# Kernel optimization log

Measured on AMD Instinct MI355X. Metric: run time of the kernel, lower is better.

Reference implementation:

```python
import jax, jax.numpy as jnp
import numpy as np

N_NODES = 50000
N_EDGES = 600000
F_IN = 128
HID = 128
N_CLASSES = 10


def _gcn_graph(edge_index, n_nodes):
    # PyG GCNConv: add self-loops, deg computed on target (col) with weight 1,
    # norm_e = deg^-1/2[src] * deg^-1/2[dst]
    src = jnp.concatenate([edge_index[0], jnp.arange(n_nodes, dtype=edge_index.dtype)])
    dst = jnp.concatenate([edge_index[1], jnp.arange(n_nodes, dtype=edge_index.dtype)])
    deg = jax.ops.segment_sum(jnp.ones_like(dst, dtype=jnp.float32), dst, num_segments=n_nodes)
    dinv = jnp.where(deg > 0, jax.lax.rsqrt(deg), 0.0)
    norm = dinv[src] * dinv[dst]  # [E+N]
    return src, dst, norm


def _gcn_layer(x, W, b, src, dst, norm, n_nodes):
    h = x @ W                      # [N, out] linear first (bias applied post-agg)
    m = h[src] * norm[:, None]     # gather + scale, [E+N, out]
    out = jax.ops.segment_sum(m, dst, num_segments=n_nodes)  # scatter-add
    return out + b


def setup_inputs() -> dict:
    key = jax.random.key(0)
    ks = jax.random.split(key, 4)
    x = jax.random.normal(ks[0], (N_NODES, F_IN), dtype=jnp.float32)
    edge_index = jax.random.randint(ks[1], (2, N_EDGES), 0, N_NODES, dtype=jnp.int64)
    # Glorot-ish init scale for weights
    W_stack = jax.random.normal(ks[2], (8, HID, HID), dtype=jnp.float32) * (1.0 / np.sqrt(HID))
    b_stack = jnp.zeros((8, HID), dtype=jnp.float32)
    W_out = jax.random.normal(ks[3], (HID, N_CLASSES), dtype=jnp.float32) * (1.0 / np.sqrt(HID))
    b_out = jnp.zeros((N_CLASSES,), dtype=jnp.float32)
    return {"x": x, "edge_index": edge_index, "W_stack": W_stack, "b_stack": b_stack,
            "W_out": W_out, "b_out": b_out}


def reference(x, edge_index, W_stack, b_stack, W_out, b_out):
    n_nodes = x.shape[0]
    src, dst, norm = _gcn_graph(edge_index, n_nodes)
    h = x
    for i in range(8):  # conv1..conv8 with ELU
        h = jax.nn.elu(_gcn_layer(h, W_stack[i], b_stack[i], src, dst, norm, n_nodes))
    # conv9: no activation
    return _gcn_layer(h, W_out, b_out, src, dst, norm, n_nodes)
```

## Files before the change

kernel.cpp:

```cpp
#include <hip/hip_runtime.h>
#include <math.h>

#define NN 50000
#define NE 600000
#define HID 128
#define NCLS 10
#define T2S 16

typedef __bf16 bf16x8 __attribute__((ext_vector_type(8)));
typedef float f32x16 __attribute__((ext_vector_type(16)));

__device__ __forceinline__ void split3(float f, ushort& h, ushort& m, ushort& l) {
    unsigned uh = __float_as_uint(f) & 0xffff0000u;
    float fm = f - __uint_as_float(uh);
    unsigned um = __float_as_uint(fm) & 0xffff0000u;
    float fl = fm - __uint_as_float(um);
    h = (ushort)(uh >> 16);
    m = (ushort)(um >> 16);
    l = (ushort)(__float_as_uint(fl) >> 16);
}


__global__ __launch_bounds__(256) void k_count(const int* __restrict__ edge,
                                               int* __restrict__ counts) {
    int e = blockIdx.x * 256 + threadIdx.x;
    if (e < NE) atomicAdd(&counts[edge[NE + e]], 1);
}

__device__ __forceinline__ int wave_incl_scan(int x, int lane) {
#pragma unroll
    for (int off = 1; off < 64; off <<= 1) {
        int y = __shfl_up(x, off, 64);
        if (lane >= off) x += y;
    }
    return x;
}

__global__ __launch_bounds__(256) void k_scan1(const int* __restrict__ counts,
                                               int* __restrict__ rowptr,
                                               int* __restrict__ bsum,
                                               float* __restrict__ dinv) {
    __shared__ int ws[4];
    int tid = threadIdx.x;
    int i = blockIdx.x * 256 + tid;
    int lane = tid & 63, wv = tid >> 6;
    int v = (i < NN) ? counts[i] : 0;
    if (i < NN) dinv[i] = rsqrtf((float)(v + 1));
    int x = wave_incl_scan(v, lane);
    if (lane == 63) ws[wv] = x;
    __syncthreads();
    int off = 0;
    for (int j = 0; j < wv; ++j) off += ws[j];
    if (i < NN) rowptr[i] = off + x - v;
    if (tid == 255) bsum[blockIdx.x] = off + x;
}

__global__ __launch_bounds__(256) void k_scan2(int* __restrict__ bsum, int n) {
    __shared__ int ws[4];
    int tid = threadIdx.x;
    int lane = tid & 63, wv = tid >> 6;
    int v = (tid < n) ? bsum[tid] : 0;
    int x = wave_incl_scan(v, lane);
    if (lane == 63) ws[wv] = x;
    __syncthreads();
    int off = 0;
    for (int j = 0; j < wv; ++j) off += ws[j];
    __syncthreads();
    if (tid < n) bsum[tid] = off + x - v;
}

__global__ __launch_bounds__(256) void k_scan3(int* __restrict__ rowptr,
                                               const int* __restrict__ bsum) {
    int i = blockIdx.x * 256 + threadIdx.x;
    if (i < NN) rowptr[i] += bsum[blockIdx.x];
    if (i == 0) rowptr[NN] = NE;
}

__global__ __launch_bounds__(256) void k_fill(const int* __restrict__ edge,
                                              const int* __restrict__ rowptr,
                                              int* __restrict__ cursor,
                                              const float* __restrict__ dinv,
                                              int2* __restrict__ csr) {
    int e = blockIdx.x * 256 + threadIdx.x;
    if (e >= NE) return;
    int s = edge[e], d = edge[NE + e];
    int slot = atomicSub(&cursor[d], 1) - 1;
    csr[rowptr[d] + slot] = make_int2(s, __float_as_int(dinv[s] * dinv[d]));
}


__global__ __launch_bounds__(256) void k_split_w(const float* __restrict__ Wst,
                                                 ushort* __restrict__ Wt4) {
    int i = blockIdx.x * 256 + threadIdx.x;
    if (i >= 8 * HID * HID) return;
    int l = i >> 14;
    int k = (i >> 7) & 127;
    int n = i & 127;
    ushort h, m, lo;
    split3(Wst[i], h, m, lo);
    int ks = k >> 4, r = k & 15;
    size_t base = ((((size_t)l * 3) * 8 + ks) * 128 + n) * 16 + r;
    const size_t pstride = (size_t)8 * 128 * 16;
    Wt4[base] = h;
    Wt4[base + pstride] = m;
    Wt4[base + 2 * pstride] = lo;
}


__global__ __launch_bounds__(256) void k_mfma_gemm(const float* __restrict__ H,
                                                   const ushort* __restrict__ Wt,
                                                   float* __restrict__ T) {
    int tid = threadIdx.x;
    int lane = tid & 63, w = tid >> 6;
    int l31 = lane & 31, lh = lane >> 5;
    int rowbase = blockIdx.x * 128;

    int grow = rowbase + w * 32 + l31;
    if (grow >= NN) grow = NN - 1;
    const float* arow = H + (size_t)grow * HID + lh * 8;
    const ushort* wbase = Wt + (size_t)l31 * 16 + lh * 8;

    f32x16 acc[4] = {};

#pragma unroll 2
    for (int s = 0; s < 8; ++s) {
        const float4* ap = (const float4*)(arow + s * 16);
        float4 f0 = ap[0], f1 = ap[1];
        float av[8] = {f0.x, f0.y, f0.z, f0.w, f1.x, f1.y, f1.z, f1.w};
        union { ushort u[8]; bf16x8 v; } ah, am, al;
#pragma unroll
        for (int q = 0; q < 8; ++q) split3(av[q], ah.u[q], am.u[q], al.u[q]);

        uint4 bf[3][4];
#pragma unroll
        for (int p = 0; p < 3; ++p)
#pragma unroll
            for (int c = 0; c < 4; ++c)
                bf[p][c] = *(const uint4*)(wbase + (((size_t)p * 8 + s) * 128 + c * 32) * 16);

#pragma unroll
        for (int c = 0; c < 4; ++c)
            acc[c] = __builtin_amdgcn_mfma_f32_32x32x16_bf16(ah.v, *(const bf16x8*)&bf[0][c], acc[c], 0, 0, 0);
#pragma unroll
        for (int c = 0; c < 4; ++c)
            acc[c] = __builtin_amdgcn_mfma_f32_32x32x16_bf16(ah.v, *(const bf16x8*)&bf[1][c], acc[c], 0, 0, 0);
#pragma unroll
        for (int c = 0; c < 4; ++c)
            acc[c] = __builtin_amdgcn_mfma_f32_32x32x16_bf16(am.v, *(const bf16x8*)&bf[0][c], acc[c], 0, 0, 0);
#pragma unroll
        for (int c = 0; c < 4; ++c)
            acc[c] = __builtin_amdgcn_mfma_f32_32x32x16_bf16(ah.v, *(const bf16x8*)&bf[2][c], acc[c], 0, 0, 0);
#pragma unroll
        for (int c = 0; c < 4; ++c)
            acc[c] = __builtin_amdgcn_mfma_f32_32x32x16_bf16(am.v, *(const bf16x8*)&bf[1][c], acc[c], 0, 0, 0);
#pragma unroll
        for (int c = 0; c < 4; ++c)
            acc[c] = __builtin_amdgcn_mfma_f32_32x32x16_bf16(al.v, *(const bf16x8*)&bf[0][c], acc[c], 0, 0, 0);
    }

#pragma unroll
    for (int c = 0; c < 4; ++c)
#pragma unroll
        for (int reg = 0; reg < 16; ++reg) {
            int r = (reg & 3) + 8 * (reg >> 2) + 4 * lh;
            int gr = rowbase + w * 32 + r;
            if (gr < NN)
                T[(size_t)gr * HID + c * 32 + l31] = acc[c][reg];
        }
}

__device__ __forceinline__ void gather_to_lds(const float* __restrict__ Tin,
                                              const int* __restrict__ rowptr,
                                              const int2* __restrict__ csr,
                                              const float* __restrict__ dinv,
                                              float4 bv, float* Hs,
                                              int rowbase, int w, int slot, int l31,
                                              int nodes_per_wave) {
    for (int i = 0; i < nodes_per_wave; ++i) {
        int lrow = w * nodes_per_wave + i;
        int node = rowbase + lrow;
        if (node >= NN) node = NN - 1;
        int beg = rowptr[node], end = rowptr[node + 1];
        float sn = dinv[node];

        float4 acc = {0.f, 0.f, 0.f, 0.f};
        if (slot == 1) {
            float4 tv = ((const float4*)(Tin + (size_t)node * HID))[l31];
            float s2 = sn * sn;
            acc.x = s2 * tv.x + bv.x;
            acc.y = s2 * tv.y + bv.y;
            acc.z = s2 * tv.z + bv.z;
            acc.w = s2 * tv.w + bv.w;
        }

        const int2 zed = make_int2(0, 0);
        int p = beg + slot;
        int2 e0 = (p < end) ? csr[p] : zed;
        int2 e1 = (p + 2 < end) ? csr[p + 2] : zed;
        int2 e2 = (p + 4 < end) ? csr[p + 4] : zed;
        int2 e3 = (p + 6 < end) ? csr[p + 6] : zed;
        for (; p < end; p += 8) {
            float4 u0 = ((const float4*)(Tin + (size_t)e0.x * HID))[l31];
            float4 u1 = ((const float4*)(Tin + (size_t)e1.x * HID))[l31];
            float4 u2 = ((const float4*)(Tin + (size_t)e2.x * HID))[l31];
            float4 u3 = ((const float4*)(Tin + (size_t)e3.x * HID))[l31];
            float w0 = __int_as_float(e0.y), w1 = __int_as_float(e1.y);
            float w2 = __int_as_float(e2.y), w3 = __int_as_float(e3.y);
            e0 = (p + 8 < end) ? csr[p + 8] : zed;
            e1 = (p + 10 < end) ? csr[p + 10] : zed;
            e2 = (p + 12 < end) ? csr[p + 12] : zed;
            e3 = (p + 14 < end) ? csr[p + 14] : zed;
            acc.x += w0 * u0.x; acc.y += w0 * u0.y; acc.z += w0 * u0.z; acc.w += w0 * u0.w;
            acc.x += w1 * u1.x; acc.y += w1 * u1.y; acc.z += w1 * u1.z; acc.w += w1 * u1.w;
            acc.x += w2 * u2.x; acc.y += w2 * u2.y; acc.z += w2 * u2.z; acc.w += w2 * u2.w;
            acc.x += w3 * u3.x; acc.y += w3 * u3.y; acc.z += w3 * u3.z; acc.w += w3 * u3.w;
        }

        acc.x += __shfl_xor(acc.x, 32, 64);
        acc.y += __shfl_xor(acc.y, 32, 64);
        acc.z += __shfl_xor(acc.z, 32, 64);
        acc.w += __shfl_xor(acc.w, 32, 64);

        if (slot == 0) {
            float4 r = acc;
            r.x = r.x > 0.f ? r.x : expm1f(r.x);
            r.y = r.y > 0.f ? r.y : expm1f(r.y);
            r.z = r.z > 0.f ? r.z : expm1f(r.z);
            r.w = r.w > 0.f ? r.w : expm1f(r.w);
            int byte = lrow * 512 + l31 * 16;
            byte ^= (lrow & 7) << 4;
            *(float4*)((char*)Hs + byte) = r;
        }
    }
}


__global__ __launch_bounds__(256) void k_fused(const float* __restrict__ Tin,
                                               const ushort* __restrict__ Wt,
                                               const int* __restrict__ rowptr,
                                               const int2* __restrict__ csr,
                                               const float* __restrict__ dinv,
                                               const float* __restrict__ bias,
                                               float* __restrict__ Tout) {
    __shared__ float Hs[32 * 128];
    int tid = threadIdx.x;
    int lane = tid & 63, w = tid >> 6;
    int slot = lane >> 5, l31 = lane & 31;
    int rowbase = blockIdx.x * 32;

    float4 bv = ((const float4*)bias)[l31];

    gather_to_lds(Tin, rowptr, csr, dinv, bv, Hs, rowbase, w, slot, l31, 8);
    __syncthreads();

    if (w >= 2) return;

    int lh = slot;
    int colh = w;
    const ushort* wbase = Wt + ((size_t)(colh * 64) + l31) * 16 + lh * 8;

    f32x16 acc2[2] = {};

#pragma unroll 2
    for (int s = 0; s < 8; ++s) {
        int byte = l31 * 512 + s * 64 + lh * 32;
        int sw = (l31 & 7) << 4;
        float4 f0 = *(const float4*)((const char*)Hs + (byte ^ sw));
        float4 f1 = *(const float4*)((const char*)Hs + ((byte + 16) ^ sw));
        float av[8] = {f0.x, f0.y, f0.z, f0.w, f1.x, f1.y, f1.z, f1.w};
        union { ushort u[8]; bf16x8 v; } ah, am, al;
#pragma unroll
        for (int q = 0; q < 8; ++q) split3(av[q], ah.u[q], am.u[q], al.u[q]);

        uint4 bf[3][2];
#pragma unroll
        for (int p = 0; p < 3; ++p)
#pragma unroll
            for (int c = 0; c < 2; ++c)
                bf[p][c] = *(const uint4*)(wbase + (((size_t)p * 8 + s) * 128 + c * 32) * 16);

#pragma unroll
        for (int c = 0; c < 2; ++c)
            acc2[c] = __builtin_amdgcn_mfma_f32_32x32x16_bf16(ah.v, *(const bf16x8*)&bf[0][c], acc2[c], 0, 0, 0);
#pragma unroll
        for (int c = 0; c < 2; ++c)
            acc2[c] = __builtin_amdgcn_mfma_f32_32x32x16_bf16(ah.v, *(const bf16x8*)&bf[1][c], acc2[c], 0, 0, 0);
#pragma unroll
        for (int c = 0; c < 2; ++c)
            acc2[c] = __builtin_amdgcn_mfma_f32_32x32x16_bf16(am.v, *(const bf16x8*)&bf[0][c], acc2[c], 0, 0, 0);
#pragma unroll
        for (int c = 0; c < 2; ++c)
            acc2[c] = __builtin_amdgcn_mfma_f32_32x32x16_bf16(ah.v, *(const bf16x8*)&bf[2][c], acc2[c], 0, 0, 0);
#pragma unroll
        for (int c = 0; c < 2; ++c)
            acc2[c] = __builtin_amdgcn_mfma_f32_32x32x16_bf16(am.v, *(const bf16x8*)&bf[1][c], acc2[c], 0, 0, 0);
#pragma unroll
        for (int c = 0; c < 2; ++c)
            acc2[c] = __builtin_amdgcn_mfma_f32_32x32x16_bf16(al.v, *(const bf16x8*)&bf[0][c], acc2[c], 0, 0, 0);
    }

#pragma unroll
    for (int c = 0; c < 2; ++c)
#pragma unroll
        for (int reg = 0; reg < 16; ++reg) {
            int r = (reg & 3) + 8 * (reg >> 2) + 4 * lh;
            int gr = rowbase + r;
            if (gr < NN)
                Tout[(size_t)gr * HID + colh * 64 + c * 32 + l31] = acc2[c][reg];
        }
}


__global__ __launch_bounds__(256) void k_fused_out(const float* __restrict__ Tin,
                                                   const float* __restrict__ W,
                                                   const int* __restrict__ rowptr,
                                                   const int2* __restrict__ csr,
                                                   const float* __restrict__ dinv,
                                                   const float* __restrict__ bias,
                                                   float* __restrict__ T2) {
    __shared__ float Hs[32 * 128];
    __shared__ float Ws[128 * 11];
    int tid = threadIdx.x;
    int lane = tid & 63, w = tid >> 6;
    int slot = lane >> 5, l31 = lane & 31;
    int rowbase = blockIdx.x * 32;

    for (int m = tid; m < HID * NCLS; m += 256) {
        int k = m / NCLS, c = m - k * NCLS;
        Ws[k * 11 + c] = W[m];
    }

    float4 bv = ((const float4*)bias)[l31];
    gather_to_lds(Tin, rowptr, csr, dinv, bv, Hs, rowbase, w, slot, l31, 8);
    __syncthreads();

    int row = tid >> 3;
    int t8 = tid & 7;
    float acc[NCLS];
#pragma unroll
    for (int c = 0; c < NCLS; ++c) acc[c] = 0.f;
    int sw = (row & 7) << 4;
    int base = row * 512 + t8 * 64;
#pragma unroll
    for (int q = 0; q < 4; ++q) {
        float4 f = *(const float4*)((const char*)Hs + ((base + q * 16) ^ sw));
        float hv[4] = {f.x, f.y, f.z, f.w};
#pragma unroll
        for (int j = 0; j < 4; ++j) {
            const float* wr = &Ws[(t8 * 16 + q * 4 + j) * 11];
#pragma unroll
            for (int c = 0; c < NCLS; ++c) acc[c] += hv[j] * wr[c];
        }
    }
#pragma unroll
    for (int off = 4; off >= 1; off >>= 1) {
#pragma unroll
        for (int c = 0; c < NCLS; ++c) acc[c] += __shfl_xor(acc[c], off, 8);
    }
    int gr = rowbase + row;
    if (t8 == 0 && gr < NN) {
#pragma unroll
        for (int c = 0; c < NCLS; ++c) T2[(size_t)gr * T2S + c] = acc[c];
    }
}

__global__ __launch_bounds__(256) void k_gather_out(const float* __restrict__ T2,
                                                    float* __restrict__ out,
                                                    const int* __restrict__ rowptr,
                                                    const int2* __restrict__ csr,
                                                    const float* __restrict__ dinv,
                                                    const float* __restrict__ bias) {
    int lane = threadIdx.x & 63;
    int node = (blockIdx.x * 256 + threadIdx.x) >> 6;
    if (node >= NN) return;
    int slot = lane >> 4, c = lane & 15;
    int beg = rowptr[node], end = rowptr[node + 1];
    float acc = 0.f;
    if (c < NCLS) {
        for (int i = beg + slot; i < end; i += 4) {
            int2 e = csr[i];
            acc += __int_as_float(e.y) * T2[(size_t)e.x * T2S + c];
        }
    }
    acc += __shfl_xor(acc, 16, 64);
    acc += __shfl_xor(acc, 32, 64);
    if (slot == 0 && c < NCLS) {
        float sn = dinv[node];
        sn *= sn;
        out[node * NCLS + c] = acc + sn * T2[(size_t)node * T2S + c] + bias[c];
    }
}


extern "C" void kernel_launch(void* const* d_in, const int* in_sizes, int n_in,
                              void* d_out, int out_size, void* d_ws, size_t ws_size,
                              hipStream_t stream) {
    (void)in_sizes; (void)n_in; (void)out_size; (void)ws_size;
    const float* x       = (const float*)d_in[0];
    const int*   edge    = (const int*)d_in[1];
    const float* W_stack = (const float*)d_in[2];
    const float* b_stack = (const float*)d_in[3];
    const float* W_out   = (const float*)d_in[4];
    const float* b_out   = (const float*)d_in[5];
    float* out = (float*)d_out;

    char* ws = (char*)d_ws;
    const size_t bigbuf = (size_t)NN * HID * sizeof(float);
    float* X      = (float*)ws;
    float* Y      = (float*)(ws + bigbuf);
    char*  p      = ws + 2 * bigbuf;
    int2*  csr    = (int2*)p;              p += sizeof(int2) * NE;
    float* dinv   = (float*)p;             p += sizeof(float) * NN;
    int*   rowptr = (int*)p;               p += sizeof(int) * (NN + 1);
    int*   counts = (int*)p;               p += sizeof(int) * NN;
    int*   bsum   = (int*)p;               p += sizeof(int) * 256;
    p = (char*)(((size_t)p + 15) & ~(size_t)15);
    ushort* Wt4 = (ushort*)p;  p += sizeof(ushort) * 8 * 3 * HID * HID;
    float* T2b  = (float*)p;   p += sizeof(float) * NN * T2S;

    const int NB_N  = (NN + 255) / 256;
    const int NB_E  = (NE + 255) / 256;
    const int NB_G  = (NN + 127) / 128;
    const int NB_F  = (NN + 31) / 32;
    const int NB_A  = (NN * 64 + 255) / 256;
    const int NB_SW = (8 * HID * HID + 255) / 256;

    hipMemsetAsync(counts, 0, sizeof(int) * NN, stream);
    k_count<<<NB_E, 256, 0, stream>>>(edge, counts);
    k_scan1<<<NB_N, 256, 0, stream>>>(counts, rowptr, bsum, dinv);
    k_scan2<<<1, 256, 0, stream>>>(bsum, NB_N);
    k_scan3<<<NB_N, 256, 0, stream>>>(rowptr, bsum);
    k_fill<<<NB_E, 256, 0, stream>>>(edge, rowptr, counts, dinv, csr);

    k_split_w<<<NB_SW, 256, 0, stream>>>(W_stack, Wt4);

    k_mfma_gemm<<<NB_G, 256, 0, stream>>>(x, Wt4, Y);

    float* cur = Y;
    float* nxt = X;
    for (int l = 0; l < 7; ++l) {
        k_fused<<<NB_F, 256, 0, stream>>>(cur, Wt4 + (size_t)(l + 1) * 3 * HID * HID,
                                          rowptr, csr, dinv,
                                          b_stack + (size_t)l * HID, nxt);
        float* t = cur; cur = nxt; nxt = t;
    }

    k_fused_out<<<NB_F, 256, 0, stream>>>(cur, W_out, rowptr, csr, dinv,
                                          b_stack + (size_t)7 * HID, T2b);

    k_gather_out<<<NB_A, 256, 0, stream>>>(T2b, out, rowptr, csr, dinv, b_out);
}
```

Baseline: 693.8 us.

## Gather two nodes per wave with prefetch; 64-row tiles using all four waves for MFMA

The gather changes from splitting each node's edges across two half-waves to processing two nodes per wave, one per half-wave. This removes the cross-half shuffle reduction and the idle half during the ELU and LDS store. The next node's rowptr, dinv and self feature row are prefetched while the current node is processed. Blocks now cover 64 rows, so all four waves do MFMA work instead of two returning early. The tail projection kernel is remapped to 4 threads per row. Doubling the LDS tile and adding a launch-bounds occupancy hint may raise register pressure, and per-half-wave edge counts now diverge.

```diff
diff --git a/kernel.cpp b/kernel.cpp
--- a/kernel.cpp
+++ b/kernel.cpp
@@ -169,102 +169,105 @@
         }
 }
 
-__device__ __forceinline__ void gather_to_lds(const float* __restrict__ Tin,
-                                              const int* __restrict__ rowptr,
-                                              const int2* __restrict__ csr,
-                                              const float* __restrict__ dinv,
-                                              float4 bv, float* Hs,
-                                              int rowbase, int w, int slot, int l31,
-                                              int nodes_per_wave) {
-    for (int i = 0; i < nodes_per_wave; ++i) {
-        int lrow = w * nodes_per_wave + i;
-        int node = rowbase + lrow;
-        if (node >= NN) node = NN - 1;
-        int beg = rowptr[node], end = rowptr[node + 1];
-        float sn = dinv[node];
-
-        float4 acc = {0.f, 0.f, 0.f, 0.f};
-        if (slot == 1) {
-            float4 tv = ((const float4*)(Tin + (size_t)node * HID))[l31];
-            float s2 = sn * sn;
-            acc.x = s2 * tv.x + bv.x;
-            acc.y = s2 * tv.y + bv.y;
-            acc.z = s2 * tv.z + bv.z;
-            acc.w = s2 * tv.w + bv.w;
-        }
+__device__ __forceinline__ void gather2_to_lds(const float* __restrict__ Tin,
+                                               const int* __restrict__ rowptr,
+                                               const int2* __restrict__ csr,
+                                               const float* __restrict__ dinv,
+                                               float4 bv, float* Hs,
+                                               int rowbase, int w, int h, int l31) {
+    int lrow = w * 16 + h;
+    int node = rowbase + lrow;
+    if (node >= NN) node = NN - 1;
+    int beg = rowptr[node], end = rowptr[node + 1];
+    float sn = dinv[node];
+    float4 tv = ((const float4*)(Tin + (size_t)node * HID))[l31];
+
+    for (int i = 0; i < 8; ++i) {
+        int nlrow = lrow + 2;
+        int nbeg = 0, nend = 0;
+        float nsn = 0.f;
+        float4 ntv = {0.f, 0.f, 0.f, 0.f};
+        if (i < 7) {
+            int nnode = rowbase + nlrow;
+            if (nnode >= NN) nnode = NN - 1;
+            nbeg = rowptr[nnode];
+            nend = rowptr[nnode + 1];
+            nsn = dinv[nnode];
+            ntv = ((const float4*)(Tin + (size_t)nnode * HID))[l31];
+        }
+
+        float s2 = sn * sn;
+        float4 acc;
+        acc.x = s2 * tv.x + bv.x;
+        acc.y = s2 * tv.y + bv.y;
+        acc.z = s2 * tv.z + bv.z;
+        acc.w = s2 * tv.w + bv.w;
 
         const int2 zed = make_int2(0, 0);
-        int p = beg + slot;
+        int p = beg;
         int2 e0 = (p < end) ? csr[p] : zed;
-        int2 e1 = (p + 2 < end) ? csr[p + 2] : zed;
-        int2 e2 = (p + 4 < end) ? csr[p + 4] : zed;
-        int2 e3 = (p + 6 < end) ? csr[p + 6] : zed;
-        for (; p < end; p += 8) {
+        int2 e1 = (p + 1 < end) ? csr[p + 1] : zed;
+        int2 e2 = (p + 2 < end) ? csr[p + 2] : zed;
+        int2 e3 = (p + 3 < end) ? csr[p + 3] : zed;
+        for (; p < end; p += 4) {
             float4 u0 = ((const float4*)(Tin + (size_t)e0.x * HID))[l31];
             float4 u1 = ((const float4*)(Tin + (size_t)e1.x * HID))[l31];
             float4 u2 = ((const float4*)(Tin + (size_t)e2.x * HID))[l31];
             float4 u3 = ((const float4*)(Tin + (size_t)e3.x * HID))[l31];
             float w0 = __int_as_float(e0.y), w1 = __int_as_float(e1.y);
             float w2 = __int_as_float(e2.y), w3 = __int_as_float(e3.y);
-            e0 = (p + 8 < end) ? csr[p + 8] : zed;
-            e1 = (p + 10 < end) ? csr[p + 10] : zed;
-            e2 = (p + 12 < end) ? csr[p + 12] : zed;
-            e3 = (p + 14 < end) ? csr[p + 14] : zed;
+            e0 = (p + 4 < end) ? csr[p + 4] : zed;
+            e1 = (p + 5 < end) ? csr[p + 5] : zed;
+            e2 = (p + 6 < end) ? csr[p + 6] : zed;
+            e3 = (p + 7 < end) ? csr[p + 7] : zed;
             acc.x += w0 * u0.x; acc.y += w0 * u0.y; acc.z += w0 * u0.z; acc.w += w0 * u0.w;
             acc.x += w1 * u1.x; acc.y += w1 * u1.y; acc.z += w1 * u1.z; acc.w += w1 * u1.w;
             acc.x += w2 * u2.x; acc.y += w2 * u2.y; acc.z += w2 * u2.z; acc.w += w2 * u2.w;
             acc.x += w3 * u3.x; acc.y += w3 * u3.y; acc.z += w3 * u3.z; acc.w += w3 * u3.w;
         }
 
-        acc.x += __shfl_xor(acc.x, 32, 64);
-        acc.y += __shfl_xor(acc.y, 32, 64);
-        acc.z += __shfl_xor(acc.z, 32, 64);
-        acc.w += __shfl_xor(acc.w, 32, 64);
-
-        if (slot == 0) {
-            float4 r = acc;
-            r.x = r.x > 0.f ? r.x : expm1f(r.x);
-            r.y = r.y > 0.f ? r.y : expm1f(r.y);
-            r.z = r.z > 0.f ? r.z : expm1f(r.z);
-            r.w = r.w > 0.f ? r.w : expm1f(r.w);
-            int byte = lrow * 512 + l31 * 16;
-            byte ^= (lrow & 7) << 4;
-            *(float4*)((char*)Hs + byte) = r;
-        }
-    }
-}
-
-
-__global__ __launch_bounds__(256) void k_fused(const float* __restrict__ Tin,
-                                               const ushort* __restrict__ Wt,
-                                               const int* __restrict__ rowptr,
-                                               const int2* __restrict__ csr,
-                                               const float* __restrict__ dinv,
-                                               const float* __restrict__ bias,
-                                               float* __restrict__ Tout) {
-    __shared__ float Hs[32 * 128];
+        acc.x = acc.x > 0.f ? acc.x : expm1f(acc.x);
+        acc.y = acc.y > 0.f ? acc.y : expm1f(acc.y);
+        acc.z = acc.z > 0.f ? acc.z : expm1f(acc.z);
+        acc.w = acc.w > 0.f ? acc.w : expm1f(acc.w);
+        int byte = lrow * 512 + l31 * 16;
+        byte ^= (lrow & 7) << 4;
+        *(float4*)((char*)Hs + byte) = acc;
+
+        lrow = nlrow; beg = nbeg; end = nend; sn = nsn; tv = ntv;
+    }
+}
+
+
+__global__ __launch_bounds__(256, 4) void k_fused(const float* __restrict__ Tin,
+                                                  const ushort* __restrict__ Wt,
+                                                  const int* __restrict__ rowptr,
+                                                  const int2* __restrict__ csr,
+                                                  const float* __restrict__ dinv,
+                                                  const float* __restrict__ bias,
+                                                  float* __restrict__ Tout) {
+    __shared__ float Hs[64 * 128];
     int tid = threadIdx.x;
     int lane = tid & 63, w = tid >> 6;
-    int slot = lane >> 5, l31 = lane & 31;
-    int rowbase = blockIdx.x * 32;
+    int hh = lane >> 5, l31 = lane & 31;
+    int rowbase = blockIdx.x * 64;
 
     float4 bv = ((const float4*)bias)[l31];
 
-    gather_to_lds(Tin, rowptr, csr, dinv, bv, Hs, rowbase, w, slot, l31, 8);
+    gather2_to_lds(Tin, rowptr, csr, dinv, bv, Hs, rowbase, w, hh, l31);
     __syncthreads();
 
-    if (w >= 2) return;
-
-    int lh = slot;
-    int colh = w;
+    int lh = hh;
+    int rloc = (w >> 1) * 32 + l31;
+    int colh = w & 1;
     const ushort* wbase = Wt + ((size_t)(colh * 64) + l31) * 16 + lh * 8;
 
     f32x16 acc2[2] = {};
 
 #pragma unroll 2
     for (int s = 0; s < 8; ++s) {
-        int byte = l31 * 512 + s * 64 + lh * 32;
-        int sw = (l31 & 7) << 4;
+        int byte = rloc * 512 + s * 64 + lh * 32;
+        int sw = (rloc & 7) << 4;
         float4 f0 = *(const float4*)((const char*)Hs + (byte ^ sw));
         float4 f1 = *(const float4*)((const char*)Hs + ((byte + 16) ^ sw));
         float av[8] = {f0.x, f0.y, f0.z, f0.w, f1.x, f1.y, f1.z, f1.w};
@@ -304,26 +307,26 @@
 #pragma unroll
         for (int reg = 0; reg < 16; ++reg) {
             int r = (reg & 3) + 8 * (reg >> 2) + 4 * lh;
-            int gr = rowbase + r;
+            int gr = rowbase + (w >> 1) * 32 + r;
             if (gr < NN)
                 Tout[(size_t)gr * HID + colh * 64 + c * 32 + l31] = acc2[c][reg];
         }
 }
 
 
-__global__ __launch_bounds__(256) void k_fused_out(const float* __restrict__ Tin,
-                                                   const float* __restrict__ W,
-                                                   const int* __restrict__ rowptr,
-                                                   const int2* __restrict__ csr,
-                                                   const float* __restrict__ dinv,
-                                                   const float* __restrict__ bias,
-                                                   float* __restrict__ T2) {
-    __shared__ float Hs[32 * 128];
+__global__ __launch_bounds__(256, 4) void k_fused_out(const float* __restrict__ Tin,
+                                                      const float* __restrict__ W,
+                                                      const int* __restrict__ rowptr,
+                                                      const int2* __restrict__ csr,
+                                                      const float* __restrict__ dinv,
+                                                      const float* __restrict__ bias,
+                                                      float* __restrict__ T2) {
+    __shared__ float Hs[64 * 128];
     __shared__ float Ws[128 * 11];
     int tid = threadIdx.x;
     int lane = tid & 63, w = tid >> 6;
-    int slot = lane >> 5, l31 = lane & 31;
-    int rowbase = blockIdx.x * 32;
+    int hh = lane >> 5, l31 = lane & 31;
+    int rowbase = blockIdx.x * 64;
 
     for (int m = tid; m < HID * NCLS; m += 256) {
         int k = m / NCLS, c = m - k * NCLS;
@@ -331,34 +334,34 @@
     }
 
     float4 bv = ((const float4*)bias)[l31];
-    gather_to_lds(Tin, rowptr, csr, dinv, bv, Hs, rowbase, w, slot, l31, 8);
+    gather2_to_lds(Tin, rowptr, csr, dinv, bv, Hs, rowbase, w, hh, l31);
     __syncthreads();
 
-    int row = tid >> 3;
-    int t8 = tid & 7;
+    int row = tid >> 2;
+    int t4 = tid & 3;
     float acc[NCLS];
 #pragma unroll
     for (int c = 0; c < NCLS; ++c) acc[c] = 0.f;
     int sw = (row & 7) << 4;
-    int base = row * 512 + t8 * 64;
-#pragma unroll
-    for (int q = 0; q < 4; ++q) {
-        float4 f = *(const float4*)((const char*)Hs + ((base + q * 16) ^ sw));
+#pragma unroll
+    for (int q = 0; q < 8; ++q) {
+        int c16 = q * 4 + t4;
+        float4 f = *(const float4*)((const char*)Hs + ((row * 512 + c16 * 16) ^ sw));
         float hv[4] = {f.x, f.y, f.z, f.w};
 #pragma unroll
         for (int j = 0; j < 4; ++j) {
-            const float* wr = &Ws[(t8 * 16 + q * 4 + j) * 11];
+            const float* wr = &Ws[(c16 * 4 + j) * 11];
 #pragma unroll
             for (int c = 0; c < NCLS; ++c) acc[c] += hv[j] * wr[c];
         }
     }
 #pragma unroll
-    for (int off = 4; off >= 1; off >>= 1) {
-#pragma unroll
-        for (int c = 0; c < NCLS; ++c) acc[c] += __shfl_xor(acc[c], off, 8);
+    for (int off = 2; off >= 1; off >>= 1) {
+#pragma unroll
+        for (int c = 0; c < NCLS; ++c) acc[c] += __shfl_xor(acc[c], off, 4);
     }
     int gr = rowbase + row;
-    if (t8 == 0 && gr < NN) {
+    if (t4 == 0 && gr < NN) {
 #pragma unroll
         for (int c = 0; c < NCLS; ++c) T2[(size_t)gr * T2S + c] = acc[c];
     }
@@ -421,7 +424,7 @@
     const int NB_N  = (NN + 255) / 256;
     const int NB_E  = (NE + 255) / 256;
     const int NB_G  = (NN + 127) / 128;
-    const int NB_F  = (NN + 31) / 32;
+    const int NB_F  = (NN + 63) / 64;
     const int NB_A  = (NN * 64 + 255) / 256;
     const int NB_SW = (8 * HID * HID + 255) / 256;
 
```

Measured after the change: 649.6 us (median of 2 runs). 6.4% less time.
